# Kernel tuning notes

Hardware: AMD Instinct MI355X
Metric: run time of the kernel (lower is better)

## Reference

```python
import jax, jax.numpy as jnp
import numpy as np

E = 8          # num routed experts
TOP_K = 2      # experts per token
SCALE = 1.0    # routed_scaling_factor


def _swiglu(x, wg, wu, wd):
    # x: [T, D]; wg, wu: [H, D]; wd: [D, H]
    gate = jax.nn.silu(x @ wg.T)
    up = x @ wu.T
    return (gate * up) @ wd.T


def setup_inputs() -> dict:
    key = jax.random.key(0)
    ks = jax.random.split(key, 8)
    B, L, D, H = 2, 2048, 1024, 2048
    s = 0.02  # init scale for weights
    return {
        "x": jax.random.normal(ks[0], (B, L, D), jnp.float32),
        "gate_w": jax.random.normal(ks[1], (E, D), jnp.float32) * s,
        "sh_gate": jax.random.normal(ks[2], (H, D), jnp.float32) * s,
        "sh_up": jax.random.normal(ks[3], (H, D), jnp.float32) * s,
        "sh_down": jax.random.normal(ks[4], (D, H), jnp.float32) * s,
        "eg": jax.random.normal(ks[5], (E, H, D), jnp.float32) * s,
        "eu": jax.random.normal(ks[6], (E, H, D), jnp.float32) * s,
        "ed": jax.random.normal(ks[7], (E, D, H), jnp.float32) * s,
    }


def reference(x, gate_w, sh_gate, sh_up, sh_down, eg, eu, ed):
    B, L, D = x.shape
    T = B * L
    xf = x.reshape(T, D)

    # --- shared expert (num_shared_experts = 1, so the /1 average is identity) ---
    shared = _swiglu(xf, sh_gate, sh_up, sh_down)

    # --- MoE gate (inference mode: no jitter, no aux loss) ---
    router_logits = xf @ gate_w.T                                   # [T, E]
    router_probs = jax.nn.softmax(router_logits.astype(jnp.float32), axis=-1)
    w, idx = jax.lax.top_k(router_probs, TOP_K)                     # [T, K]
    w = w / jnp.sum(w, axis=-1, keepdims=True)
    w = w.astype(x.dtype)

    # per-token combine weights over experts: [T, E]
    comb = jnp.zeros((T, E), dtype=x.dtype).at[
        jnp.arange(T)[:, None], idx].add(w)

    # --- routed experts: dense stacked SwiGLU, zero-weight experts contribute 0 ---
    g = jax.nn.silu(jnp.einsum('td,ehd->teh', xf, eg))              # [T, E, H]
    u = jnp.einsum('td,ehd->teh', xf, eu)                           # [T, E, H]
    eo = jnp.einsum('teh,edh->ted', g * u, ed)                      # [T, E, D]
    routed = jnp.einsum('ted,te->td', eo, comb)                     # [T, D]

    out = shared + SCALE * routed
    return out.reshape(B, L, D)
```

## Files before the change

kernel.cpp:

```cpp
#include <hip/hip_runtime.h>

#define T_TOK 4096
#define DDIM  1024
#define HDIM  2048
#define NEXP  8
#define CAP   13312

typedef short bf16x8 __attribute__((ext_vector_type(8)));
typedef float f32x4  __attribute__((ext_vector_type(4)));

#define WS_XB   ((size_t)0)
#define WS_HBUF (WS_XB   + (size_t)T_TOK*DDIM*2)
#define WS_BTOK (WS_HBUF + (size_t)CAP*HDIM*2)
#define WS_BW   (WS_BTOK + (size_t)CAP*4)
#define WS_IDX  (WS_BW   + (size_t)CAP*4)
#define WS_WTOP (WS_IDX  + (size_t)2*T_TOK*4)
#define WS_CNT  (WS_WTOP + (size_t)2*T_TOK*4)
#define WS_OFF  (WS_CNT  + (size_t)64)
#define WS_END  (WS_OFF  + (size_t)64)

#define NEW_EXP ((size_t)NEXP*HDIM*DDIM)
#define NSH     ((size_t)HDIM*DDIM)
#define WS2_XB   ((size_t)0)
#define WS2_HBUF (WS2_XB   + (size_t)T_TOK*DDIM*2)
#define WS2_EGB  (WS2_HBUF + (size_t)CAP*HDIM*2)
#define WS2_EUB  (WS2_EGB  + NEW_EXP*2)
#define WS2_EDB  (WS2_EUB  + NEW_EXP*2)
#define WS2_SGB  (WS2_EDB  + NEW_EXP*2)
#define WS2_SUB  (WS2_SGB  + NSH*2)
#define WS2_SDB  (WS2_SUB  + NSH*2)
#define WS2_BTOK (WS2_SDB  + NSH*2)
#define WS2_BW   (WS2_BTOK + (size_t)CAP*4)
#define WS2_IDX  (WS2_BW   + (size_t)CAP*4)
#define WS2_WTOP (WS2_IDX  + (size_t)2*T_TOK*4)
#define WS2_CNT  (WS2_WTOP + (size_t)2*T_TOK*4)
#define WS2_OFF  (WS2_CNT  + (size_t)64)
#define WS2_ZROW (WS2_OFF  + (size_t)64)
#define WS2_END  (WS2_ZROW + (size_t)4096)

static __device__ __forceinline__ unsigned short f2bf(float f) {
  unsigned u = __float_as_uint(f);
  unsigned r = (u + 0x7FFFu + ((u >> 16) & 1u)) >> 16;
  return (unsigned short)r;
}

static __device__ __forceinline__ void gll16(const void* g, void* l) {
  __builtin_amdgcn_global_load_lds((const __attribute__((address_space(1))) void*)g,
                                   (__attribute__((address_space(3))) void*)l, 16, 0, 0);
}

__global__ __launch_bounds__(256) void k_sentinel(float* __restrict__ out) {
  int gid = blockIdx.x * 256 + threadIdx.x;
  int stride = gridDim.x * 256;
  for (int i = gid; i < T_TOK * DDIM; i += stride) out[i] = 1.0e6f;
}

__global__ __launch_bounds__(256) void k_init(float* __restrict__ out,
                                              int* __restrict__ btok,
                                              int* __restrict__ cnt,
                                              unsigned int* __restrict__ zz) {
  int gid = blockIdx.x * 256 + threadIdx.x;
  int stride = gridDim.x * 256;
  float4 z = make_float4(0.f, 0.f, 0.f, 0.f);
  for (int i = gid; i < T_TOK * DDIM / 4; i += stride) ((float4*)out)[i] = z;
  for (int i = gid; i < CAP; i += stride) btok[i] = -1;
  for (int i = gid; i < 1024; i += stride) zz[i] = 0u;
  if (gid < 16) cnt[gid] = 0;
}

#define NE8 ((long)(NEW_EXP / 8))
#define NS8 ((long)(NSH / 8))
__global__ __launch_bounds__(256) void k_convert(
    const float* __restrict__ eg, const float* __restrict__ eu, const float* __restrict__ ed,
    const float* __restrict__ sg, const float* __restrict__ su, const float* __restrict__ sd,
    unsigned short* __restrict__ egb, unsigned short* __restrict__ eub, unsigned short* __restrict__ edb,
    unsigned short* __restrict__ sgb, unsigned short* __restrict__ sub, unsigned short* __restrict__ sdb) {
  long gid = (long)blockIdx.x * 256 + threadIdx.x;
  long stride = (long)gridDim.x * 256;
  const long TOT8 = 3 * NE8 + 3 * NS8;
  for (long i = gid; i < TOT8; i += stride) {
    const float* s; unsigned short* d; long o;
    if (i < 3 * NE8) {
      long a = i >> 21, r = i & (NE8 - 1);
      s = (a == 0) ? eg : ((a == 1) ? eu : ed);
      d = (a == 0) ? egb : ((a == 1) ? eub : edb);
      o = r;
    } else {
      long b = i - 3 * NE8;
      long a = b >> 18, r = b & (NS8 - 1);
      s = (a == 0) ? sg : ((a == 1) ? su : sd);
      d = (a == 0) ? sgb : ((a == 1) ? sub : sdb);
      o = r;
    }
    float4 v0 = ((const float4*)s)[o * 2];
    float4 v1 = ((const float4*)s)[o * 2 + 1];
    ((ushort4*)d)[o * 2]     = make_ushort4(f2bf(v0.x), f2bf(v0.y), f2bf(v0.z), f2bf(v0.w));
    ((ushort4*)d)[o * 2 + 1] = make_ushort4(f2bf(v1.x), f2bf(v1.y), f2bf(v1.z), f2bf(v1.w));
  }
}

__global__ __launch_bounds__(256) void k_router(const float* __restrict__ x,
                                                const float* __restrict__ gw,
                                                unsigned short* __restrict__ xb,
                                                int* __restrict__ idx,
                                                float* __restrict__ wtop,
                                                int* __restrict__ counts) {
  int t = blockIdx.x;
  int tid = threadIdx.x;
  float4 xv = ((const float4*)(x + (size_t)t * DDIM))[tid];
  ushort4 xbv = make_ushort4(f2bf(xv.x), f2bf(xv.y), f2bf(xv.z), f2bf(xv.w));
  ((ushort4*)xb)[(size_t)t * (DDIM / 4) + tid] = xbv;

  float p[NEXP];
#pragma unroll
  for (int e = 0; e < NEXP; e++) {
    float4 g = ((const float4*)(gw + (size_t)e * DDIM))[tid];
    p[e] = xv.x * g.x + xv.y * g.y + xv.z * g.z + xv.w * g.w;
  }
#pragma unroll
  for (int e = 0; e < NEXP; e++)
    for (int off = 32; off; off >>= 1) p[e] += __shfl_down(p[e], off, 64);

  __shared__ float red[NEXP][4];
  int lane = tid & 63, wv = tid >> 6;
  if (lane == 0) {
#pragma unroll
    for (int e = 0; e < NEXP; e++) red[e][wv] = p[e];
  }
  __syncthreads();
  if (tid == 0) {
    float l[NEXP];
#pragma unroll
    for (int e = 0; e < NEXP; e++) l[e] = red[e][0] + red[e][1] + red[e][2] + red[e][3];
    int e1 = 0;
#pragma unroll
    for (int e = 1; e < NEXP; e++) if (l[e] > l[e1]) e1 = e;
    int e2 = -1;
#pragma unroll
    for (int e = 0; e < NEXP; e++) {
      if (e == e1) continue;
      if (e2 < 0 || l[e] > l[e2]) e2 = e;
    }
    float p2 = __expf(l[e2] - l[e1]);
    float s = 1.f + p2;
    idx[2 * t] = e1; idx[2 * t + 1] = e2;
    wtop[2 * t] = 1.f / s; wtop[2 * t + 1] = p2 / s;
    atomicAdd(&counts[e1], 1);
    atomicAdd(&counts[e2], 1);
  }
}

__global__ void k_offsets(const int* __restrict__ counts, int* __restrict__ off) {
  if (threadIdx.x == 0 && blockIdx.x == 0) {
    int o = 0;
    for (int e = 0; e < NEXP; e++) { off[e] = o; o += ((counts[e] + 127) >> 7) << 7; }
    off[8] = o;
    off[9] = o + T_TOK;
  }
}

__global__ __launch_bounds__(256) void k_scatter(const int* __restrict__ idx,
                                                 const float* __restrict__ wtop,
                                                 const int* __restrict__ off,
                                                 int* __restrict__ fill,
                                                 int* __restrict__ btok,
                                                 float* __restrict__ bw) {
  int t = blockIdx.x * 256 + threadIdx.x;
  if (t >= T_TOK) return;
#pragma unroll
  for (int k = 0; k < 2; k++) {
    int e = idx[2 * t + k];
    int pos = atomicAdd(&fill[e], 1);
    int d = off[e] + pos;
    btok[d] = t;
    bw[d] = wtop[2 * t + k];
  }
  int d = off[8] + t;
  btok[d] = t;
  bw[d] = 1.0f;
}


__global__ __launch_bounds__(256) void k_swiglu2(const unsigned short* __restrict__ xb,
                                                 const unsigned short* __restrict__ sgb,
                                                 const unsigned short* __restrict__ sub,
                                                 const unsigned short* __restrict__ egb,
                                                 const unsigned short* __restrict__ eub,
                                                 const int* __restrict__ off,
                                                 const int* __restrict__ btok,
                                                 const unsigned short* __restrict__ zrow,
                                                 unsigned short* __restrict__ hbuf) {
  __shared__ __align__(16) unsigned short As[128 * 64];
  __shared__ __align__(16) unsigned short Bg[64 * 64];
  __shared__ __align__(16) unsigned short Bu[64 * 64];

  int row0 = blockIdx.y * 128;
  int offv[10];
#pragma unroll
  for (int q = 0; q < 10; q++) offv[q] = off[q];
  if (row0 >= offv[9]) return;
  int e = 0;
#pragma unroll
  for (int q = 0; q < 9; q++) if (row0 >= offv[q + 1]) e = q + 1;

  const unsigned short* bgp = (e < NEXP) ? (egb + (size_t)e * HDIM * DDIM) : sgb;
  const unsigned short* bup = (e < NEXP) ? (eub + (size_t)e * HDIM * DDIM) : sub;
  int n0 = blockIdx.x * 64;
  int tid = threadIdx.x;
  int w = tid >> 6, l = tid & 63;
  int lr = l >> 3;
  int c  = (l & 7) ^ lr;

  const unsigned short* asrc[4];
#pragma unroll
  for (int j = 0; j < 4; j++) {
    int tok = btok[row0 + w * 32 + j * 8 + lr];
    asrc[j] = ((tok >= 0) ? (xb + (size_t)tok * DDIM) : zrow) + c * 8;
  }
  const unsigned short* bgsrc[2];
  const unsigned short* busrc[2];
#pragma unroll
  for (int j = 0; j < 2; j++) {
    int rb = w * 16 + j * 8 + lr;
    bgsrc[j] = bgp + (size_t)(n0 + rb) * DDIM + c * 8;
    busrc[j] = bup + (size_t)(n0 + rb) * DDIM + c * 8;
  }

  int wm = w >> 1, wn = w & 1;
  int fr = l & 15, fq = l >> 4;
  int f7 = fr & 7;

  f32x4 accG[4][2] = {};
  f32x4 accU[4][2] = {};

  for (int kt = 0; kt < DDIM / 64; kt++) {
    int ko = kt * 64;
#pragma unroll
    for (int j = 0; j < 4; j++)
      gll16(asrc[j] + ko, As + (w * 32 + j * 8) * 64);
#pragma unroll
    for (int j = 0; j < 2; j++) {
      gll16(bgsrc[j] + ko, Bg + (w * 16 + j * 8) * 64);
      gll16(busrc[j] + ko, Bu + (w * 16 + j * 8) * 64);
    }
    __syncthreads();
#pragma unroll
    for (int ks = 0; ks < 2; ks++) {
      int ck = ks * 4 + fq;
      bf16x8 a[4], bgf[2], buf_[2];
#pragma unroll
      for (int i = 0; i < 4; i++)
        a[i] = *(const bf16x8*)&As[(wm * 64 + i * 16 + fr) * 64 + ((ck ^ f7) * 8)];
#pragma unroll
      for (int j = 0; j < 2; j++) {
        bgf[j]  = *(const bf16x8*)&Bg[(wn * 32 + j * 16 + fr) * 64 + ((ck ^ f7) * 8)];
        buf_[j] = *(const bf16x8*)&Bu[(wn * 32 + j * 16 + fr) * 64 + ((ck ^ f7) * 8)];
      }
#pragma unroll
      for (int i = 0; i < 4; i++)
#pragma unroll
        for (int j = 0; j < 2; j++) {
          accG[i][j] = __builtin_amdgcn_mfma_f32_16x16x32_bf16(a[i], bgf[j], accG[i][j], 0, 0, 0);
          accU[i][j] = __builtin_amdgcn_mfma_f32_16x16x32_bf16(a[i], buf_[j], accU[i][j], 0, 0, 0);
        }
    }
    __syncthreads();
  }

#pragma unroll
  for (int i = 0; i < 4; i++)
#pragma unroll
    for (int j = 0; j < 2; j++)
#pragma unroll
      for (int r = 0; r < 4; r++) {
        float g = accG[i][j][r], u = accU[i][j][r];
        float h = g / (1.f + __expf(-g)) * u;
        int row = row0 + wm * 64 + i * 16 + fq * 4 + r;
        int col = n0 + wn * 32 + j * 16 + fr;
        hbuf[(size_t)row * HDIM + col] = f2bf(h);
      }
}

__global__ __launch_bounds__(256) void k_down2(const unsigned short* __restrict__ hbuf,
                                               const unsigned short* __restrict__ sdb,
                                               const unsigned short* __restrict__ edb,
                                               const int* __restrict__ off,
                                               const int* __restrict__ btok,
                                               const float* __restrict__ bw,
                                               float* __restrict__ out) {
  __shared__ __align__(16) unsigned short As[128 * 64];
  __shared__ __align__(16) unsigned short Bs[128 * 64];

  int row0 = blockIdx.y * 128;
  int offv[10];
#pragma unroll
  for (int q = 0; q < 10; q++) offv[q] = off[q];
  if (row0 >= offv[9]) return;
  int e = 0;
#pragma unroll
  for (int q = 0; q < 9; q++) if (row0 >= offv[q + 1]) e = q + 1;

  const unsigned short* bd = (e < NEXP) ? (edb + (size_t)e * DDIM * HDIM) : sdb;
  int n0 = blockIdx.x * 128;
  int tid = threadIdx.x;
  int w = tid >> 6, l = tid & 63;
  int lr = l >> 3;
  int c  = (l & 7) ^ lr;

  const unsigned short* asrc[4];
  const unsigned short* bsrc[4];
#pragma unroll
  for (int j = 0; j < 4; j++) {
    int r = (w * 4 + j) * 8 + lr;
    asrc[j] = hbuf + (size_t)(row0 + r) * HDIM + c * 8;
    bsrc[j] = bd   + (size_t)(n0 + r) * HDIM + c * 8;
  }

  int wm = w >> 1, wn = w & 1;
  int fr = l & 15, fq = l >> 4;
  int f7 = fr & 7;

  f32x4 acc[4][4] = {};

  for (int kt = 0; kt < HDIM / 64; kt++) {
    int ko = kt * 64;
#pragma unroll
    for (int j = 0; j < 4; j++) {
      gll16(asrc[j] + ko, As + (w * 4 + j) * 8 * 64);
      gll16(bsrc[j] + ko, Bs + (w * 4 + j) * 8 * 64);
    }
    __syncthreads();
#pragma unroll
    for (int ks = 0; ks < 2; ks++) {
      int ck = ks * 4 + fq;
      bf16x8 a[4], b[4];
#pragma unroll
      for (int i = 0; i < 4; i++)
        a[i] = *(const bf16x8*)&As[(wm * 64 + i * 16 + fr) * 64 + ((ck ^ f7) * 8)];
#pragma unroll
      for (int j = 0; j < 4; j++)
        b[j] = *(const bf16x8*)&Bs[(wn * 64 + j * 16 + fr) * 64 + ((ck ^ f7) * 8)];
#pragma unroll
      for (int i = 0; i < 4; i++)
#pragma unroll
        for (int j = 0; j < 4; j++)
          acc[i][j] = __builtin_amdgcn_mfma_f32_16x16x32_bf16(a[i], b[j], acc[i][j], 0, 0, 0);
    }
    __syncthreads();
  }

#pragma unroll
  for (int i = 0; i < 4; i++)
#pragma unroll
    for (int r = 0; r < 4; r++) {
      int brow = row0 + wm * 64 + i * 16 + fq * 4 + r;
      int tok = btok[brow];
      if (tok < 0) continue;
      float wgt = bw[brow];
#pragma unroll
      for (int j = 0; j < 4; j++) {
        int col = n0 + wn * 64 + j * 16 + fr;
        atomicAdd(&out[(size_t)tok * DDIM + col], wgt * acc[i][j][r]);
      }
    }
}

__global__ __launch_bounds__(256) void k_swiglu(const unsigned short* __restrict__ xb,
                                                const float* __restrict__ sh_gate,
                                                const float* __restrict__ sh_up,
                                                const float* __restrict__ eg,
                                                const float* __restrict__ eu,
                                                const int* __restrict__ off,
                                                const int* __restrict__ btok,
                                                unsigned short* __restrict__ hbuf) {
  __shared__ unsigned short As[128 * 72];
  __shared__ unsigned short Bg[64 * 72];
  __shared__ unsigned short Bu[64 * 72];

  int row0 = blockIdx.y * 128;
  int offv[10];
#pragma unroll
  for (int q = 0; q < 10; q++) offv[q] = off[q];
  if (row0 >= offv[9]) return;
  int e = 0;
#pragma unroll
  for (int q = 0; q < 9; q++) if (row0 >= offv[q + 1]) e = q + 1;

  const float* bgp;
  const float* bup;
  if (e < NEXP) {
    bgp = eg + (size_t)e * HDIM * DDIM;
    bup = eu + (size_t)e * HDIM * DDIM;
  } else {
    bgp = sh_gate;
    bup = sh_up;
  }
  int n0 = blockIdx.x * 64;
  int tid = threadIdx.x;

  int rtok[4];
#pragma unroll
  for (int j = 0; j < 4; j++) rtok[j] = btok[row0 + j * 32 + (tid >> 3)];

  int wid = tid >> 6, lane = tid & 63;
  int wm = wid >> 1, wn = wid & 1;
  int fr = lane & 15, fq = lane >> 4;

  f32x4 accG[4][2] = {};
  f32x4 accU[4][2] = {};

  for (int kt = 0; kt < DDIM / 64; kt++) {
#pragma unroll
    for (int j = 0; j < 4; j++) {
      int r = j * 32 + (tid >> 3), cc = tid & 7;
      uint4 v = make_uint4(0, 0, 0, 0);
      if (rtok[j] >= 0)
        v = *(const uint4*)(xb + (size_t)rtok[j] * DDIM + kt * 64 + cc * 8);
      *(uint4*)&As[r * 72 + cc * 8] = v;
    }
#pragma unroll
    for (int j = 0; j < 4; j++) {
      int q = j * 256 + tid;
      int rb = q >> 4, cc = q & 15;
      float4 vg = *(const float4*)(bgp + (size_t)(n0 + rb) * DDIM + kt * 64 + cc * 4);
      float4 vu = *(const float4*)(bup + (size_t)(n0 + rb) * DDIM + kt * 64 + cc * 4);
      *(ushort4*)&Bg[rb * 72 + cc * 4] = make_ushort4(f2bf(vg.x), f2bf(vg.y), f2bf(vg.z), f2bf(vg.w));
      *(ushort4*)&Bu[rb * 72 + cc * 4] = make_ushort4(f2bf(vu.x), f2bf(vu.y), f2bf(vu.z), f2bf(vu.w));
    }
    __syncthreads();
#pragma unroll
    for (int ks = 0; ks < 2; ks++) {
      bf16x8 a[4], bgf[2], buf_[2];
#pragma unroll
      for (int i = 0; i < 4; i++)
        a[i] = *(const bf16x8*)&As[(wm * 64 + i * 16 + fr) * 72 + ks * 32 + fq * 8];
#pragma unroll
      for (int j = 0; j < 2; j++) {
        bgf[j]  = *(const bf16x8*)&Bg[(wn * 32 + j * 16 + fr) * 72 + ks * 32 + fq * 8];
        buf_[j] = *(const bf16x8*)&Bu[(wn * 32 + j * 16 + fr) * 72 + ks * 32 + fq * 8];
      }
#pragma unroll
      for (int i = 0; i < 4; i++)
#pragma unroll
        for (int j = 0; j < 2; j++) {
          accG[i][j] = __builtin_amdgcn_mfma_f32_16x16x32_bf16(a[i], bgf[j], accG[i][j], 0, 0, 0);
          accU[i][j] = __builtin_amdgcn_mfma_f32_16x16x32_bf16(a[i], buf_[j], accU[i][j], 0, 0, 0);
        }
    }
    __syncthreads();
  }

#pragma unroll
  for (int i = 0; i < 4; i++)
#pragma unroll
    for (int j = 0; j < 2; j++)
#pragma unroll
      for (int r = 0; r < 4; r++) {
        float g = accG[i][j][r], u = accU[i][j][r];
        float h = g / (1.f + __expf(-g)) * u;
        int row = row0 + wm * 64 + i * 16 + fq * 4 + r;
        int col = n0 + wn * 32 + j * 16 + fr;
        hbuf[(size_t)row * HDIM + col] = f2bf(h);
      }
}

__global__ __launch_bounds__(256) void k_down(const unsigned short* __restrict__ hbuf,
                                              const float* __restrict__ sh_down,
                                              const float* __restrict__ ed,
                                              const int* __restrict__ off,
                                              const int* __restrict__ btok,
                                              const float* __restrict__ bw,
                                              float* __restrict__ out) {
  __shared__ unsigned short As[128 * 72];
  __shared__ unsigned short Bs[128 * 72];

  int row0 = blockIdx.y * 128;
  int offv[10];
#pragma unroll
  for (int q = 0; q < 10; q++) offv[q] = off[q];
  if (row0 >= offv[9]) return;
  int e = 0;
#pragma unroll
  for (int q = 0; q < 9; q++) if (row0 >= offv[q + 1]) e = q + 1;

  const float* bd = (e < NEXP) ? (ed + (size_t)e * DDIM * HDIM) : sh_down;
  int n0 = blockIdx.x * 128;
  int tid = threadIdx.x;
  int wid = tid >> 6, lane = tid & 63;
  int wm = wid >> 1, wn = wid & 1;
  int fr = lane & 15, fq = lane >> 4;

  f32x4 acc[4][4] = {};

  for (int kt = 0; kt < HDIM / 64; kt++) {
#pragma unroll
    for (int j = 0; j < 4; j++) {
      int r = j * 32 + (tid >> 3), cc = tid & 7;
      *(uint4*)&As[r * 72 + cc * 8] =
          *(const uint4*)(hbuf + (size_t)(row0 + r) * HDIM + kt * 64 + cc * 8);
    }
#pragma unroll
    for (int j = 0; j < 8; j++) {
      int q = j * 256 + tid;
      int rb = q >> 4, cc = q & 15;
      float4 v = *(const float4*)(bd + (size_t)(n0 + rb) * HDIM + kt * 64 + cc * 4);
      *(ushort4*)&Bs[rb * 72 + cc * 4] = make_ushort4(f2bf(v.x), f2bf(v.y), f2bf(v.z), f2bf(v.w));
    }
    __syncthreads();
#pragma unroll
    for (int ks = 0; ks < 2; ks++) {
      bf16x8 a[4], b[4];
#pragma unroll
      for (int i = 0; i < 4; i++)
        a[i] = *(const bf16x8*)&As[(wm * 64 + i * 16 + fr) * 72 + ks * 32 + fq * 8];
#pragma unroll
      for (int j = 0; j < 4; j++)
        b[j] = *(const bf16x8*)&Bs[(wn * 64 + j * 16 + fr) * 72 + ks * 32 + fq * 8];
#pragma unroll
      for (int i = 0; i < 4; i++)
#pragma unroll
        for (int j = 0; j < 4; j++)
          acc[i][j] = __builtin_amdgcn_mfma_f32_16x16x32_bf16(a[i], b[j], acc[i][j], 0, 0, 0);
    }
    __syncthreads();
  }

#pragma unroll
  for (int i = 0; i < 4; i++)
#pragma unroll
    for (int r = 0; r < 4; r++) {
      int brow = row0 + wm * 64 + i * 16 + fq * 4 + r;
      int tok = btok[brow];
      if (tok < 0) continue;
      float w = bw[brow];
#pragma unroll
      for (int j = 0; j < 4; j++) {
        int col = n0 + wn * 64 + j * 16 + fr;
        atomicAdd(&out[(size_t)tok * DDIM + col], w * acc[i][j][r]);
      }
    }
}

extern "C" void kernel_launch(void* const* d_in, const int* in_sizes, int n_in,
                              void* d_out, int out_size, void* d_ws, size_t ws_size,
                              hipStream_t stream) {
  const float* x       = (const float*)d_in[0];
  const float* gw      = (const float*)d_in[1];
  const float* sh_gate = (const float*)d_in[2];
  const float* sh_up   = (const float*)d_in[3];
  const float* sh_down = (const float*)d_in[4];
  const float* eg      = (const float*)d_in[5];
  const float* eu      = (const float*)d_in[6];
  const float* ed      = (const float*)d_in[7];
  float* out = (float*)d_out;
  char* ws = (char*)d_ws;

  if (ws_size >= WS2_END) {
    unsigned short* xb   = (unsigned short*)(ws + WS2_XB);
    unsigned short* hbuf = (unsigned short*)(ws + WS2_HBUF);
    unsigned short* egb  = (unsigned short*)(ws + WS2_EGB);
    unsigned short* eub  = (unsigned short*)(ws + WS2_EUB);
    unsigned short* edb  = (unsigned short*)(ws + WS2_EDB);
    unsigned short* sgb  = (unsigned short*)(ws + WS2_SGB);
    unsigned short* sub  = (unsigned short*)(ws + WS2_SUB);
    unsigned short* sdb  = (unsigned short*)(ws + WS2_SDB);
    int*   btok  = (int*)(ws + WS2_BTOK);
    float* bw    = (float*)(ws + WS2_BW);
    int*   idx   = (int*)(ws + WS2_IDX);
    float* wtop  = (float*)(ws + WS2_WTOP);
    int*   cnt   = (int*)(ws + WS2_CNT);
    int*   fill  = cnt + 8;
    int*   off   = (int*)(ws + WS2_OFF);
    unsigned short* zrow = (unsigned short*)(ws + WS2_ZROW);

    hipLaunchKernelGGL(k_init,    dim3(2048), dim3(256), 0, stream, out, btok, cnt, (unsigned int*)zrow);
    hipLaunchKernelGGL(k_convert, dim3(2048), dim3(256), 0, stream,
                       eg, eu, ed, sh_gate, sh_up, sh_down, egb, eub, edb, sgb, sub, sdb);
    hipLaunchKernelGGL(k_router,  dim3(T_TOK), dim3(256), 0, stream, x, gw, xb, idx, wtop, cnt);
    hipLaunchKernelGGL(k_offsets, dim3(1), dim3(64), 0, stream, cnt, off);
    hipLaunchKernelGGL(k_scatter, dim3(T_TOK / 256), dim3(256), 0, stream, idx, wtop, off, fill, btok, bw);
    hipLaunchKernelGGL(k_swiglu2, dim3(HDIM / 64, CAP / 128), dim3(256), 0, stream,
                       xb, sgb, sub, egb, eub, off, btok, zrow, hbuf);
    hipLaunchKernelGGL(k_down2,   dim3(DDIM / 128, CAP / 128), dim3(256), 0, stream,
                       hbuf, sdb, edb, off, btok, bw, out);
  } else if (ws_size >= WS_END) {
    unsigned short* xb   = (unsigned short*)(ws + WS_XB);
    unsigned short* hbuf = (unsigned short*)(ws + WS_HBUF);
    int*   btok  = (int*)(ws + WS_BTOK);
    float* bw    = (float*)(ws + WS_BW);
    int*   idx   = (int*)(ws + WS_IDX);
    float* wtop  = (float*)(ws + WS_WTOP);
    int*   cnt   = (int*)(ws + WS_CNT);
    int*   fill  = cnt + 8;
    int*   off   = (int*)(ws + WS_OFF);

    hipLaunchKernelGGL(k_init,    dim3(2048), dim3(256), 0, stream, out, btok, cnt, (unsigned int*)xb);
    hipLaunchKernelGGL(k_router,  dim3(T_TOK), dim3(256), 0, stream, x, gw, xb, idx, wtop, cnt);
    hipLaunchKernelGGL(k_offsets, dim3(1), dim3(64), 0, stream, cnt, off);
    hipLaunchKernelGGL(k_scatter, dim3(T_TOK / 256), dim3(256), 0, stream, idx, wtop, off, fill, btok, bw);
    hipLaunchKernelGGL(k_swiglu,  dim3(HDIM / 64, CAP / 128), dim3(256), 0, stream,
                       xb, sh_gate, sh_up, eg, eu, off, btok, hbuf);
    hipLaunchKernelGGL(k_down,    dim3(DDIM / 128, CAP / 128), dim3(256), 0, stream,
                       hbuf, sh_down, ed, off, btok, bw, out);
  } else {
    hipLaunchKernelGGL(k_sentinel, dim3(1024), dim3(256), 0, stream, out);
  }
}
```

Baseline: 680.5 us.

## Double-buffer LDS tiles in MoE GEMMs and split weight conversion per tensor

Both expert GEMM kernels (gate/up SwiGLU and down projection) now use two LDS buffers. The next K-tile's global-to-LDS loads are issued before the MFMA work on the current tile, which removes one barrier per iteration and overlaps load latency with compute. The weight conversion kernel now uses a 2D grid with one grid row per tensor, so the per-element branch selecting source and destination goes away. This doubles LDS use per block, which may lower occupancy, and the shared-weight rows of the conversion grid get far less work than the expert rows.

```diff
diff --git a/kernel.cpp b/kernel.cpp
--- a/kernel.cpp
+++ b/kernel.cpp
@@ -75,27 +75,21 @@
     const float* __restrict__ sg, const float* __restrict__ su, const float* __restrict__ sd,
     unsigned short* __restrict__ egb, unsigned short* __restrict__ eub, unsigned short* __restrict__ edb,
     unsigned short* __restrict__ sgb, unsigned short* __restrict__ sub, unsigned short* __restrict__ sdb) {
+  int a = blockIdx.y;
+  const float* s; unsigned short* d; long n8;
+  if      (a == 0) { s = eg; d = egb; n8 = NE8; }
+  else if (a == 1) { s = eu; d = eub; n8 = NE8; }
+  else if (a == 2) { s = ed; d = edb; n8 = NE8; }
+  else if (a == 3) { s = sg; d = sgb; n8 = NS8; }
+  else if (a == 4) { s = su; d = sub; n8 = NS8; }
+  else             { s = sd; d = sdb; n8 = NS8; }
   long gid = (long)blockIdx.x * 256 + threadIdx.x;
   long stride = (long)gridDim.x * 256;
-  const long TOT8 = 3 * NE8 + 3 * NS8;
-  for (long i = gid; i < TOT8; i += stride) {
-    const float* s; unsigned short* d; long o;
-    if (i < 3 * NE8) {
-      long a = i >> 21, r = i & (NE8 - 1);
-      s = (a == 0) ? eg : ((a == 1) ? eu : ed);
-      d = (a == 0) ? egb : ((a == 1) ? eub : edb);
-      o = r;
-    } else {
-      long b = i - 3 * NE8;
-      long a = b >> 18, r = b & (NS8 - 1);
-      s = (a == 0) ? sg : ((a == 1) ? su : sd);
-      d = (a == 0) ? sgb : ((a == 1) ? sub : sdb);
-      o = r;
-    }
-    float4 v0 = ((const float4*)s)[o * 2];
-    float4 v1 = ((const float4*)s)[o * 2 + 1];
-    ((ushort4*)d)[o * 2]     = make_ushort4(f2bf(v0.x), f2bf(v0.y), f2bf(v0.z), f2bf(v0.w));
-    ((ushort4*)d)[o * 2 + 1] = make_ushort4(f2bf(v1.x), f2bf(v1.y), f2bf(v1.z), f2bf(v1.w));
+  for (long i = gid; i < n8; i += stride) {
+    float4 v0 = ((const float4*)s)[i * 2];
+    float4 v1 = ((const float4*)s)[i * 2 + 1];
+    ((ushort4*)d)[i * 2]     = make_ushort4(f2bf(v0.x), f2bf(v0.y), f2bf(v0.z), f2bf(v0.w));
+    ((ushort4*)d)[i * 2 + 1] = make_ushort4(f2bf(v1.x), f2bf(v1.y), f2bf(v1.z), f2bf(v1.w));
   }
 }
 
@@ -190,9 +184,9 @@
                                                  const int* __restrict__ btok,
                                                  const unsigned short* __restrict__ zrow,
                                                  unsigned short* __restrict__ hbuf) {
-  __shared__ __align__(16) unsigned short As[128 * 64];
-  __shared__ __align__(16) unsigned short Bg[64 * 64];
-  __shared__ __align__(16) unsigned short Bu[64 * 64];
+  __shared__ __align__(16) unsigned short As[2][128 * 64];
+  __shared__ __align__(16) unsigned short Bg[2][64 * 64];
+  __shared__ __align__(16) unsigned short Bu[2][64 * 64];
 
   int row0 = blockIdx.y * 128;
   int offv[10];
@@ -233,28 +227,32 @@
   f32x4 accG[4][2] = {};
   f32x4 accU[4][2] = {};
 
+#define SW_STAGE(buf, kt) do { int ko_ = (kt) * 64;                            \
+    _Pragma("unroll")                                                          \
+    for (int j = 0; j < 4; j++)                                                \
+      gll16(asrc[j] + ko_, &As[buf][(w * 32 + j * 8) * 64]);                   \
+    _Pragma("unroll")                                                          \
+    for (int j = 0; j < 2; j++) {                                              \
+      gll16(bgsrc[j] + ko_, &Bg[buf][(w * 16 + j * 8) * 64]);                  \
+      gll16(busrc[j] + ko_, &Bu[buf][(w * 16 + j * 8) * 64]);                  \
+    } } while (0)
+
+  SW_STAGE(0, 0);
+  __syncthreads();
+  int cur = 0;
   for (int kt = 0; kt < DDIM / 64; kt++) {
-    int ko = kt * 64;
-#pragma unroll
-    for (int j = 0; j < 4; j++)
-      gll16(asrc[j] + ko, As + (w * 32 + j * 8) * 64);
-#pragma unroll
-    for (int j = 0; j < 2; j++) {
-      gll16(bgsrc[j] + ko, Bg + (w * 16 + j * 8) * 64);
-      gll16(busrc[j] + ko, Bu + (w * 16 + j * 8) * 64);
-    }
-    __syncthreads();
+    if (kt < DDIM / 64 - 1) SW_STAGE(cur ^ 1, kt + 1);
 #pragma unroll
     for (int ks = 0; ks < 2; ks++) {
       int ck = ks * 4 + fq;
       bf16x8 a[4], bgf[2], buf_[2];
 #pragma unroll
       for (int i = 0; i < 4; i++)
-        a[i] = *(const bf16x8*)&As[(wm * 64 + i * 16 + fr) * 64 + ((ck ^ f7) * 8)];
+        a[i] = *(const bf16x8*)&As[cur][(wm * 64 + i * 16 + fr) * 64 + ((ck ^ f7) * 8)];
 #pragma unroll
       for (int j = 0; j < 2; j++) {
-        bgf[j]  = *(const bf16x8*)&Bg[(wn * 32 + j * 16 + fr) * 64 + ((ck ^ f7) * 8)];
-        buf_[j] = *(const bf16x8*)&Bu[(wn * 32 + j * 16 + fr) * 64 + ((ck ^ f7) * 8)];
+        bgf[j]  = *(const bf16x8*)&Bg[cur][(wn * 32 + j * 16 + fr) * 64 + ((ck ^ f7) * 8)];
+        buf_[j] = *(const bf16x8*)&Bu[cur][(wn * 32 + j * 16 + fr) * 64 + ((ck ^ f7) * 8)];
       }
 #pragma unroll
       for (int i = 0; i < 4; i++)
@@ -265,7 +263,9 @@
         }
     }
     __syncthreads();
-  }
+    cur ^= 1;
+  }
+#undef SW_STAGE
 
 #pragma unroll
   for (int i = 0; i < 4; i++)
@@ -288,8 +288,8 @@
                                                const int* __restrict__ btok,
                                                const float* __restrict__ bw,
                                                float* __restrict__ out) {
-  __shared__ __align__(16) unsigned short As[128 * 64];
-  __shared__ __align__(16) unsigned short Bs[128 * 64];
+  __shared__ __align__(16) unsigned short As[2][128 * 64];
+  __shared__ __align__(16) unsigned short Bs[2][128 * 64];
 
   int row0 = blockIdx.y * 128;
   int offv[10];
@@ -322,24 +322,28 @@
 
   f32x4 acc[4][4] = {};
 
+#define DN_STAGE(buf, kt) do { int ko_ = (kt) * 64;                            \
+    _Pragma("unroll")                                                          \
+    for (int j = 0; j < 4; j++) {                                              \
+      gll16(asrc[j] + ko_, &As[buf][(w * 4 + j) * 8 * 64]);                    \
+      gll16(bsrc[j] + ko_, &Bs[buf][(w * 4 + j) * 8 * 64]);                    \
+    } } while (0)
+
+  DN_STAGE(0, 0);
+  __syncthreads();
+  int cur = 0;
   for (int kt = 0; kt < HDIM / 64; kt++) {
-    int ko = kt * 64;
-#pragma unroll
-    for (int j = 0; j < 4; j++) {
-      gll16(asrc[j] + ko, As + (w * 4 + j) * 8 * 64);
-      gll16(bsrc[j] + ko, Bs + (w * 4 + j) * 8 * 64);
-    }
-    __syncthreads();
+    if (kt < HDIM / 64 - 1) DN_STAGE(cur ^ 1, kt + 1);
 #pragma unroll
     for (int ks = 0; ks < 2; ks++) {
       int ck = ks * 4 + fq;
       bf16x8 a[4], b[4];
 #pragma unroll
       for (int i = 0; i < 4; i++)
-        a[i] = *(const bf16x8*)&As[(wm * 64 + i * 16 + fr) * 64 + ((ck ^ f7) * 8)];
+        a[i] = *(const bf16x8*)&As[cur][(wm * 64 + i * 16 + fr) * 64 + ((ck ^ f7) * 8)];
 #pragma unroll
       for (int j = 0; j < 4; j++)
-        b[j] = *(const bf16x8*)&Bs[(wn * 64 + j * 16 + fr) * 64 + ((ck ^ f7) * 8)];
+        b[j] = *(const bf16x8*)&Bs[cur][(wn * 64 + j * 16 + fr) * 64 + ((ck ^ f7) * 8)];
 #pragma unroll
       for (int i = 0; i < 4; i++)
 #pragma unroll
@@ -347,7 +351,9 @@
           acc[i][j] = __builtin_amdgcn_mfma_f32_16x16x32_bf16(a[i], b[j], acc[i][j], 0, 0, 0);
     }
     __syncthreads();
-  }
+    cur ^= 1;
+  }
+#undef DN_STAGE
 
 #pragma unroll
   for (int i = 0; i < 4; i++)
@@ -574,7 +580,7 @@
     unsigned short* zrow = (unsigned short*)(ws + WS2_ZROW);
 
     hipLaunchKernelGGL(k_init,    dim3(2048), dim3(256), 0, stream, out, btok, cnt, (unsigned int*)zrow);
-    hipLaunchKernelGGL(k_convert, dim3(2048), dim3(256), 0, stream,
+    hipLaunchKernelGGL(k_convert, dim3(1024, 6), dim3(256), 0, stream,
                        eg, eu, ed, sh_gate, sh_up, sh_down, egb, eub, edb, sgb, sub, sdb);
     hipLaunchKernelGGL(k_router,  dim3(T_TOK), dim3(256), 0, stream, x, gw, xb, idx, wtop, cnt);
     hipLaunchKernelGGL(k_offsets, dim3(1), dim3(64), 0, stream, cnt, off);
```

Result: no change. 690.5 us (+1.5%).
